# Kernel optimization log

Hardware: AMD Instinct MI355X
Metric: run time of the kernel (lower is better)

The kernel has to match this reference:

```python
import jax, jax.numpy as jnp
import numpy as np
import math

NUM_HEADS = 16
HIDDEN = 1024
MLP = 4096
SEQ = 2048
HEAD_DIM = HIDDEN // NUM_HEADS  # 64
EPS = 1e-5


def setup_inputs() -> dict:
    key = jax.random.key(0)
    ks = jax.random.split(key, 16)
    s = 0.02
    inp = {
        "x": jax.random.normal(ks[0], (SEQ, HIDDEN), jnp.float32),
        "rope_cos": jnp.cos(jnp.arange(SEQ, dtype=jnp.float32)[:, None] * (1.0 / (10000.0 ** (jnp.arange(HEAD_DIM // 2, dtype=jnp.float32) * 2 / HEAD_DIM)))[None, :]),
        "rope_sin": jnp.sin(jnp.arange(SEQ, dtype=jnp.float32)[:, None] * (1.0 / (10000.0 ** (jnp.arange(HEAD_DIM // 2, dtype=jnp.float32) * 2 / HEAD_DIM)))[None, :]),
        "norm0_w": jnp.ones((HIDDEN,), jnp.float32),
        "norm0_b": jnp.zeros((HIDDEN,), jnp.float32),
        "norm1_w": jnp.ones((HIDDEN,), jnp.float32),
        "norm1_b": jnp.zeros((HIDDEN,), jnp.float32),
        "wqkv_w": jax.random.normal(ks[1], (3 * HIDDEN, HIDDEN), jnp.float32) * s,
        "wqkv_b": jnp.zeros((3 * HIDDEN,), jnp.float32),
        "wo_w": jax.random.normal(ks[2], (HIDDEN, HIDDEN), jnp.float32) * s,
        "wo_b": jnp.zeros((HIDDEN,), jnp.float32),
        "up_w": jax.random.normal(ks[3], (MLP, HIDDEN), jnp.float32) * s,
        "up_b": jnp.zeros((MLP,), jnp.float32),
        "down_w": jax.random.normal(ks[4], (HIDDEN, MLP), jnp.float32) * s,
        "down_b": jnp.zeros((HIDDEN,), jnp.float32),
        # 4 packed sequences of length 512 each
        "input_row_offsets": jnp.array([0, 512, 1024, 1536, 2048], jnp.int32),
    }
    return inp


def _layernorm(x, w, b):
    m = jnp.mean(x, axis=-1, keepdims=True)
    v = jnp.mean((x - m) ** 2, axis=-1, keepdims=True)
    return (x - m) * jax.lax.rsqrt(v + EPS) * w + b


def _rope(t, cos, sin):
    # t: [S, nh, hd]; cos/sin: [S, hd/2] -> complex rotation of adjacent pairs
    S, nh, hd = t.shape
    t2 = t.reshape(S, nh, hd // 2, 2)
    re, im = t2[..., 0], t2[..., 1]
    c = cos[:, None, :]
    s = sin[:, None, :]
    out = jnp.stack([re * c - im * s, re * s + im * c], axis=-1)
    return out.reshape(S, nh, hd)


def _block(x, rope_cos, rope_sin, norm0_w, norm0_b, wqkv_w, wqkv_b, wo_w, wo_b,
           up_w, up_b, down_w, down_b, norm1_w, norm1_b, input_row_offsets):
    S, H = x.shape
    nh, hd = NUM_HEADS, HEAD_DIM
    h = _layernorm(x, norm0_w, norm0_b)
    qkv = (h @ wqkv_w.T + wqkv_b).reshape(S, 3, nh, hd)
    q, k, v = qkv[:, 0], qkv[:, 1], qkv[:, 2]
    q = _rope(q, rope_cos, rope_sin)
    k = _rope(k, rope_cos, rope_sin)
    # block-diagonal bool mask added as 0/1 float (matches torch `attn_weight += bool_mask`)
    seg = jnp.searchsorted(input_row_offsets, jnp.arange(S), side="right") - 1
    mask = (seg[:, None] == seg[None, :]).astype(jnp.float32)  # [S, S]
    scores = jnp.einsum("shd,thd->hst", q, k) / math.sqrt(hd) + mask[None]
    attn = jax.nn.softmax(scores.astype(jnp.float32), axis=-1).astype(q.dtype)
    out = jnp.einsum("hst,thd->shd", attn, v).reshape(S, H)
    x = x + (out @ wo_w.T + wo_b)
    h = _layernorm(x, norm1_w, norm1_b)
    h = jax.nn.gelu(h @ up_w.T + up_b, approximate=True)
    return x + (h @ down_w.T + down_b)


def reference(x, rope_cos, rope_sin, norm0_w, norm0_b, norm1_w, norm1_b,
              wqkv_w, wqkv_b, wo_w, wo_b, up_w, up_b, down_w, down_b,
              input_row_offsets):
    return _block(x, rope_cos, rope_sin, norm0_w, norm0_b, wqkv_w, wqkv_b,
                  wo_w, wo_b, up_w, up_b, down_w, down_b, norm1_w, norm1_b,
                  input_row_offsets)
```

## Files before the change

kernel.cpp:

```cpp
#include <hip/hip_runtime.h>
#include <hip/hip_bf16.h>
#include <math.h>

#define SEQ 2048
#define HID 1024
#define NH 16
#define HD 64

using f32x4  = __attribute__((ext_vector_type(4))) float;
using bf16x8 = __attribute__((ext_vector_type(8))) short;

union U8 { unsigned int u[4]; bf16x8 v; short s[8]; };

__device__ __forceinline__ short f2bf(float f) {
  unsigned int x = __float_as_uint(f);
  unsigned int r = (x + 0x7fffu + ((x >> 16) & 1u)) >> 16;
  return (short)(r & 0xffffu);
}

__device__ __forceinline__ unsigned int pkbf(float a, float b) {
  return ((unsigned int)(unsigned short)f2bf(a)) |
         (((unsigned int)(unsigned short)f2bf(b)) << 16);
}

__device__ __forceinline__ float bf2f_lo(unsigned int u) {
  return __uint_as_float((u & 0xffffu) << 16);
}
__device__ __forceinline__ float bf2f_hi(unsigned int u) {
  return __uint_as_float(u & 0xffff0000u);
}

__device__ __forceinline__ float fast_exp2(float x) {
#if __has_builtin(__builtin_amdgcn_exp2f)
  return __builtin_amdgcn_exp2f(x);
#else
  return exp2f(x);
#endif
}

__device__ __forceinline__ float fast_rcp(float x) {
#if __has_builtin(__builtin_amdgcn_rcpf)
  return __builtin_amdgcn_rcpf(x);
#else
  return 1.0f / x;
#endif
}

__device__ __forceinline__ void async_cp16(const void* g, void* l) {
  __builtin_amdgcn_global_load_lds(
      (__attribute__((address_space(1))) void*)(g),
      (__attribute__((address_space(3))) void*)(l), 16, 0, 0);
}

__global__ void cvt_all_kernel(const float* __restrict__ a, const float* __restrict__ b,
                               const float* __restrict__ c, const float* __restrict__ d,
                               short* __restrict__ oa, short* __restrict__ ob,
                               short* __restrict__ oc, short* __restrict__ od) {
  int i = blockIdx.x * blockDim.x + threadIdx.x;
  const float* src; short* dst; int off;
  if (i < 786432)        { src = a; dst = oa; off = i; }
  else if (i < 1048576)  { src = b; dst = ob; off = i - 786432; }
  else if (i < 2097152)  { src = c; dst = oc; off = i - 1048576; }
  else                   { src = d; dst = od; off = i - 2097152; }
  float4 v = ((const float4*)src)[off];
  short4 o;
  o.x = f2bf(v.x); o.y = f2bf(v.y); o.z = f2bf(v.z); o.w = f2bf(v.w);
  ((short4*)dst)[off] = o;
}

__global__ __launch_bounds__(256) void ln_kernel(const float* __restrict__ x,
    const float* __restrict__ w, const float* __restrict__ b, short* __restrict__ out) {
  int row = blockIdx.x;
  int tid = threadIdx.x;
  float4 v = ((const float4*)(x + (size_t)row * HID))[tid];
  float s  = v.x + v.y + v.z + v.w;
  float s2 = v.x*v.x + v.y*v.y + v.z*v.z + v.w*v.w;
#pragma unroll
  for (int o = 32; o >= 1; o >>= 1) {
    s  += __shfl_xor(s,  o);
    s2 += __shfl_xor(s2, o);
  }
  __shared__ float red[8];
  int wv = tid >> 6;
  if ((tid & 63) == 0) { red[wv] = s; red[4 + wv] = s2; }
  __syncthreads();
  float ts  = red[0] + red[1] + red[2] + red[3];
  float ts2 = red[4] + red[5] + red[6] + red[7];
  float mean = ts * (1.0f / HID);
  float var  = ts2 * (1.0f / HID) - mean * mean;
  float rs = rsqrtf(var + 1e-5f);
  float4 wv4 = ((const float4*)w)[tid];
  float4 bv4 = ((const float4*)b)[tid];
  short4 o;
  o.x = f2bf((v.x - mean) * rs * wv4.x + bv4.x);
  o.y = f2bf((v.y - mean) * rs * wv4.y + bv4.y);
  o.z = f2bf((v.z - mean) * rs * wv4.z + bv4.z);
  o.w = f2bf((v.w - mean) * rs * wv4.w + bv4.w);
  ((short4*)(out + (size_t)row * HID))[tid] = o;
}

__global__ __launch_bounds__(256) void ropev_kernel(const short* __restrict__ qkvb,
    const float* __restrict__ cosb, const float* __restrict__ sinb,
    short* __restrict__ Qh, short* __restrict__ Kh, short* __restrict__ Vt) {
  __shared__ short tile[64 * 72];
  int s0   = blockIdx.x * 64;
  int head = blockIdx.y;
  int tid  = threadIdx.x;
#pragma unroll
  for (int p = 0; p < 2; p++) {
    int seg = p * 256 + tid;
    int row = seg >> 3;
    int c8  = seg & 7;
    bf16x8 v = *(const bf16x8*)(qkvb + (size_t)(s0 + row) * 3072 + 2048 + head * 64 + c8 * 8);
    *(bf16x8*)(tile + row * 72 + c8 * 8) = v;
  }
  int sl = tid >> 3;
  int c  = tid & 7;
#pragma unroll
  for (int j = 0; j < 2; j++) {
    float scale = (j == 0) ? 0.18033688011112043f : 1.0f;
    short* dstm = (j == 0) ? Qh : Kh;
#pragma unroll
    for (int half = 0; half < 2; half++) {
      int s = s0 + half * 32 + sl;
      uint4 uu = *(const uint4*)(qkvb + (size_t)s * 3072 + j * 1024 + head * 64 + c * 8);
      float4 cs = *(const float4*)(cosb + s * 32 + c * 4);
      float4 sn = *(const float4*)(sinb + s * 32 + c * 4);
      uint4 oo;
      {
        float a = bf2f_lo(uu.x), b = bf2f_hi(uu.x);
        oo.x = pkbf(scale * (a * cs.x - b * sn.x), scale * (a * sn.x + b * cs.x));
        a = bf2f_lo(uu.y); b = bf2f_hi(uu.y);
        oo.y = pkbf(scale * (a * cs.y - b * sn.y), scale * (a * sn.y + b * cs.y));
        a = bf2f_lo(uu.z); b = bf2f_hi(uu.z);
        oo.z = pkbf(scale * (a * cs.z - b * sn.z), scale * (a * sn.z + b * cs.z));
        a = bf2f_lo(uu.w); b = bf2f_hi(uu.w);
        oo.w = pkbf(scale * (a * cs.w - b * sn.w), scale * (a * sn.w + b * cs.w));
      }
      *(uint4*)(dstm + ((size_t)head * SEQ + s) * HD + c * 8) = oo;
    }
  }
  __syncthreads();
#pragma unroll
  for (int p = 0; p < 2; p++) {
    int seg = p * 256 + tid;
    int d   = seg >> 3;
    int sc  = seg & 7;
    U8 o;
#pragma unroll
    for (int jj = 0; jj < 8; jj++) o.s[jj] = tile[(sc * 8 + jj) * 72 + d];
    *(bf16x8*)(Vt + ((size_t)head * HD + d) * SEQ + s0 + sc * 8) = o.v;
  }
}

template <int EPI>
__global__ __launch_bounds__(256) void gemm_bt_kernel(
    const short* __restrict__ A, const short* __restrict__ B,
    const float* __restrict__ bias, const float* __restrict__ resid,
    void* __restrict__ outp, int M, int N, int Klen, int Kstride) {
  __shared__ __attribute__((aligned(16))) short Alds[2 * 128 * 64];
  __shared__ __attribute__((aligned(16))) short Blds[2 * 128 * 64];
  int tid = threadIdx.x;
  int w    = tid >> 6;
  int lane = tid & 63;
  int lcol  = lane & 15;
  int lhalf = lane >> 4;
  int m0 = blockIdx.y * 128;
  int n0 = blockIdx.x * 128;
  int z  = blockIdx.z;
  int wm = (w & 1) * 64;
  int wn = (w >> 1) * 64;

  const short* apt[4];
  const short* bpt[4];
#pragma unroll
  for (int p = 0; p < 4; p++) {
    int seg = p * 256 + tid;
    int row = seg >> 3;
    int c   = (seg & 7) ^ (row & 7);
    apt[p] = A + (size_t)z * Klen + (size_t)(m0 + row) * Kstride + c * 8;
    bpt[p] = B + (size_t)z * Klen + (size_t)(n0 + row) * Kstride + c * 8;
  }

  f32x4 acc[4][4];
#pragma unroll
  for (int i = 0; i < 4; i++)
#pragma unroll
    for (int j = 0; j < 4; j++) acc[i][j] = (f32x4){0.f, 0.f, 0.f, 0.f};

  int nk = Klen >> 6;

#pragma unroll
  for (int p = 0; p < 4; p++) {
    async_cp16(apt[p], Alds + p * 2048 + w * 512);  apt[p] += 64;
    async_cp16(bpt[p], Blds + p * 2048 + w * 512);  bpt[p] += 64;
  }

  for (int kt = 0; kt < nk; ++kt) {
    int cur = kt & 1;
    const short* Ab = Alds + cur * 8192;
    const short* Bb = Blds + cur * 8192;
    if (kt + 1 < nk) {
      int nb = (cur ^ 1) * 8192;
#pragma unroll
      for (int p = 0; p < 4; p++) {
        async_cp16(apt[p], Alds + nb + p * 2048 + w * 512);  apt[p] += 64;
        async_cp16(bpt[p], Blds + nb + p * 2048 + w * 512);  bpt[p] += 64;
      }
      asm volatile("s_waitcnt vmcnt(8)" ::: "memory");
    } else {
      asm volatile("s_waitcnt vmcnt(0)" ::: "memory");
    }
    __builtin_amdgcn_s_barrier();
    __builtin_amdgcn_sched_barrier(0);
#pragma unroll
    for (int kc = 0; kc < 2; kc++) {
      bf16x8 af[4], bfr[4];
#pragma unroll
      for (int i = 0; i < 4; i++) {
        int row = wm + i * 16 + lcol;
        af[i] = *(const bf16x8*)(Ab + row * 64 + (((kc * 4 + lhalf) ^ (row & 7)) * 8));
      }
#pragma unroll
      for (int j = 0; j < 4; j++) {
        int row = wn + j * 16 + lcol;
        bfr[j] = *(const bf16x8*)(Bb + row * 64 + (((kc * 4 + lhalf) ^ (row & 7)) * 8));
      }
#pragma unroll
      for (int i = 0; i < 4; i++)
#pragma unroll
        for (int j = 0; j < 4; j++)
          acc[i][j] = __builtin_amdgcn_mfma_f32_16x16x32_bf16(af[i], bfr[j], acc[i][j], 0, 0, 0);
    }
    __builtin_amdgcn_s_barrier();
    __builtin_amdgcn_sched_barrier(0);
  }

#pragma unroll
  for (int i = 0; i < 4; i++) {
#pragma unroll
    for (int j = 0; j < 4; j++) {
#pragma unroll
      for (int r = 0; r < 4; r++) {
        int row = m0 + wm + i * 16 + lhalf * 4 + r;
        int col = n0 + wn + j * 16 + lcol;
        float v = acc[i][j][r];
        if (EPI != 5) v += bias[col];
        if (EPI == 2) {
          float t = v * (1.5957691216057308f + 0.07135481283942279f * v * v);
          float e = fast_exp2(t * -1.4426950408889634f);
          v = v * fast_rcp(1.0f + e);
          ((short*)outp)[(size_t)row * N + col] = f2bf(v);
        } else if (EPI == 3) {
          ((short*)outp)[(size_t)row * N + col] = f2bf(v);
        } else {
          ((short*)outp)[(size_t)z * M * N + (size_t)row * N + col] = f2bf(v);
        }
      }
    }
  }
}

__global__ __launch_bounds__(256) void attn_kernel(
    const short* __restrict__ Qh, const short* __restrict__ Kh,
    const short* __restrict__ Vt, const int* __restrict__ offs,
    short* __restrict__ Opart, float* __restrict__ Lpart) {
  __shared__ __attribute__((aligned(16))) short Klds[64 * 64];
  __shared__ __attribute__((aligned(16))) short Vlds[64 * 64];
  __shared__ __attribute__((aligned(16))) unsigned int Plds[4][16 * 34];
  int head = blockIdx.y;
  int q0   = blockIdx.x * 64;
  int z    = blockIdx.z;
  int tid  = threadIdx.x;
  int w    = tid >> 6;
  int lane = tid & 63;
  int lcol = lane & 15;
  int h    = lane >> 4;
  int s7   = lcol & 7;
  int o1 = offs[1], o2 = offs[2], o3 = offs[3];

  int qrow = q0 + w * 16 + lcol;
  const short* qb = Qh + ((size_t)head * SEQ + qrow) * HD;
  bf16x8 qf0 = *(const bf16x8*)(qb + h * 8);
  bf16x8 qf1 = *(const bf16x8*)(qb + 32 + h * 8);
  int sq = (qrow >= o1) + (qrow >= o2) + (qrow >= o3);
  U8 qe;
  qe.u[0] = 0; qe.u[1] = 0; qe.u[2] = 0; qe.u[3] = 0;
  if (h == 0) qe.s[sq] = (short)0x3FB9;

  bf16x8 ones;
#pragma unroll
  for (int i = 0; i < 8; i++) ones[i] = 0x3F80;

  int kb0 = lcol * 64 + ((h ^ s7) * 8);
  int kb1 = lcol * 64 + (((4 + h) ^ s7) * 8);
  int vb0 = kb0, vb1 = kb1;
  int pwb = lcol * 34 + h * 2;
  int prb = lcol * 34 + h * 4;

  int tbeg = z * 512;
  const short* kp0; const short* kp1; const short* vp0; const short* vp1;
  {
    int seg = tid, row = seg >> 3, g = (seg & 7) ^ (row & 7);
    kp0 = Kh + ((size_t)head * SEQ + tbeg + row) * HD + g * 8;
    vp0 = Vt + ((size_t)head * HD + row) * SEQ + tbeg + g * 8;
    seg = 256 + tid; row = seg >> 3; g = (seg & 7) ^ (row & 7);
    kp1 = Kh + ((size_t)head * SEQ + tbeg + row) * HD + g * 8;
    vp1 = Vt + ((size_t)head * HD + row) * SEQ + tbeg + g * 8;
  }

  f32x4 o_acc[4];
#pragma unroll
  for (int nt = 0; nt < 4; nt++) o_acc[nt] = (f32x4){0.f, 0.f, 0.f, 0.f};
  f32x4 acc_l = (f32x4){0.f, 0.f, 0.f, 0.f};

  for (int t0 = 0; t0 < 512; t0 += 64) {
    async_cp16(kp0, Klds + w * 512);          kp0 += 64 * HD;
    async_cp16(kp1, Klds + 2048 + w * 512);   kp1 += 64 * HD;
    async_cp16(vp0, Vlds + w * 512);          vp0 += 64;
    async_cp16(vp1, Vlds + 2048 + w * 512);   vp1 += 64;
    __syncthreads();

#pragma unroll
    for (int n = 0; n < 4; n++) {
      bf16x8 kf0 = *(const bf16x8*)(Klds + n * 1024 + kb0);
      bf16x8 kf1 = *(const bf16x8*)(Klds + n * 1024 + kb1);
      int key = tbeg + t0 + n * 16 + lcol;
      int sk = (key >= o1) + (key >= o2) + (key >= o3);
      U8 ke;
      ke.u[0] = (h == 0) ? ((sk == 0) ? 0x00003F80u : (sk == 1) ? 0x3F800000u : 0u) : 0u;
      ke.u[1] = (h == 0) ? ((sk == 2) ? 0x00003F80u : (sk == 3) ? 0x3F800000u : 0u) : 0u;
      ke.u[2] = 0; ke.u[3] = 0;

      f32x4 sacc = (f32x4){0.f, 0.f, 0.f, 0.f};
      sacc = __builtin_amdgcn_mfma_f32_16x16x32_bf16(kf0, qf0, sacc, 0, 0, 0);
      sacc = __builtin_amdgcn_mfma_f32_16x16x32_bf16(kf1, qf1, sacc, 0, 0, 0);
      sacc = __builtin_amdgcn_mfma_f32_16x16x32_bf16(ke.v, qe.v, sacc, 0, 0, 0);

      float p0 = fast_exp2(sacc[0]);
      float p1 = fast_exp2(sacc[1]);
      float p2 = fast_exp2(sacc[2]);
      float p3 = fast_exp2(sacc[3]);
      uint2 pw;
      pw.x = __builtin_amdgcn_perm(__float_as_uint(p1), __float_as_uint(p0), 0x07060302);
      pw.y = __builtin_amdgcn_perm(__float_as_uint(p3), __float_as_uint(p2), 0x07060302);
      *(uint2*)&Plds[w][pwb + n * 8] = pw;
    }

#pragma unroll
    for (int kc = 0; kc < 2; kc++) {
      uint2 a = *(const uint2*)&Plds[w][prb + kc * 16];
      uint2 b = *(const uint2*)&Plds[w][prb + kc * 16 + 2];
      U8 pu;
      pu.u[0] = a.x; pu.u[1] = a.y; pu.u[2] = b.x; pu.u[3] = b.y;
      int vb = kc ? vb1 : vb0;
#pragma unroll
      for (int nt = 0; nt < 4; nt++) {
        bf16x8 vf = *(const bf16x8*)(Vlds + nt * 1024 + vb);
        o_acc[nt] = __builtin_amdgcn_mfma_f32_16x16x32_bf16(vf, pu.v, o_acc[nt], 0, 0, 0);
      }
      acc_l = __builtin_amdgcn_mfma_f32_16x16x32_bf16(ones, pu.v, acc_l, 0, 0, 0);
    }
    __syncthreads();
  }

  short* op = Opart + ((size_t)z * SEQ + qrow) * HID + head * HD + h * 4;
#pragma unroll
  for (int nt = 0; nt < 4; nt++) {
    uint2 ua;
    ua.x = pkbf(o_acc[nt][0], o_acc[nt][1]);
    ua.y = pkbf(o_acc[nt][2], o_acc[nt][3]);
    *(uint2*)(op + nt * 16) = ua;
  }
  if (lane < 16)
    Lpart[((size_t)z * NH + head) * SEQ + qrow] = acc_l[0];
}

__global__ __launch_bounds__(256) void attn_merge_kernel(
    const short* __restrict__ Opart, const float* __restrict__ Lpart,
    short* __restrict__ attn) {
  int i = blockIdx.x * blockDim.x + threadIdx.x;
  int col4 = i & 255;
  int row  = i >> 8;
  int head = col4 >> 4;
  float acc0 = 0.f, acc1 = 0.f, acc2 = 0.f, acc3 = 0.f, l = 0.f;
#pragma unroll
  for (int zz = 0; zz < 4; zz++) {
    uint2 p = ((const uint2*)(Opart + (size_t)zz * SEQ * HID))[i];
    acc0 += bf2f_lo(p.x); acc1 += bf2f_hi(p.x);
    acc2 += bf2f_lo(p.y); acc3 += bf2f_hi(p.y);
    l += Lpart[((size_t)zz * NH + head) * SEQ + row];
  }
  float rl = fast_rcp(l);
  uint2 o;
  o.x = pkbf(acc0 * rl, acc1 * rl);
  o.y = pkbf(acc2 * rl, acc3 * rl);
  ((uint2*)attn)[i] = o;
}

__global__ __launch_bounds__(256) void merge_ln_kernel(
    const short* __restrict__ part, const float* __restrict__ bias,
    const float* __restrict__ resid, const float* __restrict__ w,
    const float* __restrict__ b, float* __restrict__ x1, short* __restrict__ h1) {
  int row = blockIdx.x;
  int tid = threadIdx.x;
  size_t idx = (size_t)row * HID / 4 + tid;
  float4 v = {0.f, 0.f, 0.f, 0.f};
#pragma unroll
  for (int z = 0; z < 4; z++) {
    uint2 p = ((const uint2*)(part + (size_t)z * SEQ * HID))[idx];
    v.x += bf2f_lo(p.x); v.y += bf2f_hi(p.x);
    v.z += bf2f_lo(p.y); v.w += bf2f_hi(p.y);
  }
  float4 bi = ((const float4*)bias)[tid];
  float4 rs4 = ((const float4*)(resid + (size_t)row * HID))[tid];
  v.x += bi.x + rs4.x; v.y += bi.y + rs4.y; v.z += bi.z + rs4.z; v.w += bi.w + rs4.w;
  ((float4*)(x1 + (size_t)row * HID))[tid] = v;
  float s  = v.x + v.y + v.z + v.w;
  float s2 = v.x*v.x + v.y*v.y + v.z*v.z + v.w*v.w;
#pragma unroll
  for (int o = 32; o >= 1; o >>= 1) {
    s  += __shfl_xor(s,  o);
    s2 += __shfl_xor(s2, o);
  }
  __shared__ float red[8];
  int wv = tid >> 6;
  if ((tid & 63) == 0) { red[wv] = s; red[4 + wv] = s2; }
  __syncthreads();
  float ts  = red[0] + red[1] + red[2] + red[3];
  float ts2 = red[4] + red[5] + red[6] + red[7];
  float mean = ts * (1.0f / HID);
  float var  = ts2 * (1.0f / HID) - mean * mean;
  float rsq = rsqrtf(var + 1e-5f);
  float4 wv4 = ((const float4*)w)[tid];
  float4 bv4 = ((const float4*)b)[tid];
  short4 o;
  o.x = f2bf((v.x - mean) * rsq * wv4.x + bv4.x);
  o.y = f2bf((v.y - mean) * rsq * wv4.y + bv4.y);
  o.z = f2bf((v.z - mean) * rsq * wv4.z + bv4.z);
  o.w = f2bf((v.w - mean) * rsq * wv4.w + bv4.w);
  ((short4*)(h1 + (size_t)row * HID))[tid] = o;
}

__global__ __launch_bounds__(256) void merge_bias_kernel(
    const short* __restrict__ part, const float* __restrict__ bias,
    const float* __restrict__ resid, float* __restrict__ out) {
  int i = blockIdx.x * blockDim.x + threadIdx.x;
  int col4 = i & 255;
  float4 v = {0.f, 0.f, 0.f, 0.f};
#pragma unroll
  for (int z = 0; z < 4; z++) {
    uint2 p = ((const uint2*)(part + (size_t)z * SEQ * HID))[i];
    v.x += bf2f_lo(p.x); v.y += bf2f_hi(p.x);
    v.z += bf2f_lo(p.y); v.w += bf2f_hi(p.y);
  }
  float4 bi = ((const float4*)bias)[col4];
  float4 rs = ((const float4*)resid)[i];
  float4 o;
  o.x = v.x + bi.x + rs.x;
  o.y = v.y + bi.y + rs.y;
  o.z = v.z + bi.z + rs.z;
  o.w = v.w + bi.w + rs.w;
  ((float4*)out)[i] = o;
}

extern "C" void kernel_launch(void* const* d_in, const int* in_sizes, int n_in,
                              void* d_out, int out_size, void* d_ws, size_t ws_size,
                              hipStream_t stream) {
  const float* x      = (const float*)d_in[0];
  const float* ropec  = (const float*)d_in[1];
  const float* ropes  = (const float*)d_in[2];
  const float* n0w    = (const float*)d_in[3];
  const float* n0b    = (const float*)d_in[4];
  const float* n1w    = (const float*)d_in[5];
  const float* n1b    = (const float*)d_in[6];
  const float* wqkv_w = (const float*)d_in[7];
  const float* wqkv_b = (const float*)d_in[8];
  const float* wo_w   = (const float*)d_in[9];
  const float* wo_b   = (const float*)d_in[10];
  const float* up_w   = (const float*)d_in[11];
  const float* up_b   = (const float*)d_in[12];
  const float* down_w = (const float*)d_in[13];
  const float* down_b = (const float*)d_in[14];
  const int*   offs   = (const int*)d_in[15];
  float* out = (float*)d_out;

  char* base = (char*)d_ws;
  short* wqkv_bf = (short*)(base + 0);
  short* wo_bf   = (short*)(base + 6291456);
  short* up_bf   = (short*)(base + 8388608);
  short* down_bf = (short*)(base + 16777216);
  short* h0      = (short*)(base + 25165824);
  short* qkv_bf  = (short*)(base + 29360128);
  short* Qh      = (short*)(base + 41943040);
  short* Kh      = (short*)(base + 46137344);
  short* Vt      = (short*)(base + 50331648);
  short* Opart   = (short*)(base + 54525952);
  float* Lpart   = (float*)(base + 71303168);
  short* attn    = (short*)(base + 71827456);
  float* x1      = (float*)(base + 76021760);
  short* h1      = (short*)(base + 84410368);
  short* wopart  = (short*)(base + 25165824);
  short* u       = (short*)(base + 25165824);
  short* dnpart  = (short*)(base + 41943040);

  cvt_all_kernel<<<12288, 256, 0, stream>>>(wqkv_w, wo_w, up_w, down_w,
                                            wqkv_bf, wo_bf, up_bf, down_bf);
  ln_kernel<<<2048, 256, 0, stream>>>(x, n0w, n0b, h0);
  gemm_bt_kernel<3><<<dim3(24, 16), 256, 0, stream>>>(h0, wqkv_bf, wqkv_b, nullptr,
                                                      qkv_bf, 2048, 3072, 1024, 1024);
  ropev_kernel<<<dim3(32, 16), 256, 0, stream>>>(qkv_bf, ropec, ropes, Qh, Kh, Vt);
  attn_kernel<<<dim3(32, 16, 4), 256, 0, stream>>>(Qh, Kh, Vt, offs, Opart, Lpart);
  attn_merge_kernel<<<2048, 256, 0, stream>>>(Opart, Lpart, attn);
  gemm_bt_kernel<5><<<dim3(8, 16, 4), 256, 0, stream>>>(attn, wo_bf, nullptr, nullptr,
                                                        wopart, 2048, 1024, 256, 1024);
  merge_ln_kernel<<<2048, 256, 0, stream>>>(wopart, wo_b, x, n1w, n1b, x1, h1);
  gemm_bt_kernel<2><<<dim3(32, 16), 256, 0, stream>>>(h1, up_bf, up_b, nullptr,
                                                      u, 2048, 4096, 1024, 1024);
  gemm_bt_kernel<5><<<dim3(8, 16, 4), 256, 0, stream>>>(u, down_bf, nullptr, nullptr,
                                                        dnpart, 2048, 1024, 1024, 4096);
  merge_bias_kernel<<<2048, 256, 0, stream>>>(dnpart, down_b, x1, out);
}
```

Before: 265.5 us.

## Split-K QKV/up/down GEMMs with single-buffer LDS, fuse LN into convert kernel

Merges the weight-conversion and first layernorm into a single launch. QKV, up and down projections switch to split-K (2 or 8 ways) with a single-buffered LDS variant for higher occupancy and more blocks. Bias, GELU and rope now consume the partial sums in the follow-on kernels, and a new merge_gelu kernel is added. This trades extra bf16 partial-sum traffic and an extra launch for more parallelism and less LDS per block, and loses the copy/compute overlap of double buffering in those GEMMs.

```diff
diff --git a/kernel.cpp b/kernel.cpp
--- a/kernel.cpp
+++ b/kernel.cpp
@@ -46,17 +46,56 @@
 #endif
 }
 
+__device__ __forceinline__ float gelu_f(float v) {
+  float t = v * (1.5957691216057308f + 0.07135481283942279f * v * v);
+  float e = fast_exp2(t * -1.4426950408889634f);
+  return v * fast_rcp(1.0f + e);
+}
+
 __device__ __forceinline__ void async_cp16(const void* g, void* l) {
   __builtin_amdgcn_global_load_lds(
       (__attribute__((address_space(1))) void*)(g),
       (__attribute__((address_space(3))) void*)(l), 16, 0, 0);
 }
 
-__global__ void cvt_all_kernel(const float* __restrict__ a, const float* __restrict__ b,
-                               const float* __restrict__ c, const float* __restrict__ d,
-                               short* __restrict__ oa, short* __restrict__ ob,
-                               short* __restrict__ oc, short* __restrict__ od) {
-  int i = blockIdx.x * blockDim.x + threadIdx.x;
+__global__ __launch_bounds__(256) void cvtln_kernel(
+    const float* __restrict__ a, const float* __restrict__ b,
+    const float* __restrict__ c, const float* __restrict__ d,
+    short* __restrict__ oa, short* __restrict__ ob,
+    short* __restrict__ oc, short* __restrict__ od,
+    const float* __restrict__ x, const float* __restrict__ w,
+    const float* __restrict__ bb, short* __restrict__ h0) {
+  int tid = threadIdx.x;
+  if (blockIdx.x < 2048) {
+    int row = blockIdx.x;
+    float4 v = ((const float4*)(x + (size_t)row * HID))[tid];
+    float s  = v.x + v.y + v.z + v.w;
+    float s2 = v.x*v.x + v.y*v.y + v.z*v.z + v.w*v.w;
+#pragma unroll
+    for (int o = 32; o >= 1; o >>= 1) {
+      s  += __shfl_xor(s,  o);
+      s2 += __shfl_xor(s2, o);
+    }
+    __shared__ float red[8];
+    int wv = tid >> 6;
+    if ((tid & 63) == 0) { red[wv] = s; red[4 + wv] = s2; }
+    __syncthreads();
+    float ts  = red[0] + red[1] + red[2] + red[3];
+    float ts2 = red[4] + red[5] + red[6] + red[7];
+    float mean = ts * (1.0f / HID);
+    float var  = ts2 * (1.0f / HID) - mean * mean;
+    float rs = rsqrtf(var + 1e-5f);
+    float4 wv4 = ((const float4*)w)[tid];
+    float4 bv4 = ((const float4*)bb)[tid];
+    short4 o;
+    o.x = f2bf((v.x - mean) * rs * wv4.x + bv4.x);
+    o.y = f2bf((v.y - mean) * rs * wv4.y + bv4.y);
+    o.z = f2bf((v.z - mean) * rs * wv4.z + bv4.z);
+    o.w = f2bf((v.w - mean) * rs * wv4.w + bv4.w);
+    ((short4*)(h0 + (size_t)row * HID))[tid] = o;
+    return;
+  }
+  int i = (blockIdx.x - 2048) * 256 + tid;
   const float* src; short* dst; int off;
   if (i < 786432)        { src = a; dst = oa; off = i; }
   else if (i < 1048576)  { src = b; dst = ob; off = i - 786432; }
@@ -68,41 +107,12 @@
   ((short4*)dst)[off] = o;
 }
 
-__global__ __launch_bounds__(256) void ln_kernel(const float* __restrict__ x,
-    const float* __restrict__ w, const float* __restrict__ b, short* __restrict__ out) {
-  int row = blockIdx.x;
-  int tid = threadIdx.x;
-  float4 v = ((const float4*)(x + (size_t)row * HID))[tid];
-  float s  = v.x + v.y + v.z + v.w;
-  float s2 = v.x*v.x + v.y*v.y + v.z*v.z + v.w*v.w;
-#pragma unroll
-  for (int o = 32; o >= 1; o >>= 1) {
-    s  += __shfl_xor(s,  o);
-    s2 += __shfl_xor(s2, o);
-  }
-  __shared__ float red[8];
-  int wv = tid >> 6;
-  if ((tid & 63) == 0) { red[wv] = s; red[4 + wv] = s2; }
-  __syncthreads();
-  float ts  = red[0] + red[1] + red[2] + red[3];
-  float ts2 = red[4] + red[5] + red[6] + red[7];
-  float mean = ts * (1.0f / HID);
-  float var  = ts2 * (1.0f / HID) - mean * mean;
-  float rs = rsqrtf(var + 1e-5f);
-  float4 wv4 = ((const float4*)w)[tid];
-  float4 bv4 = ((const float4*)b)[tid];
-  short4 o;
-  o.x = f2bf((v.x - mean) * rs * wv4.x + bv4.x);
-  o.y = f2bf((v.y - mean) * rs * wv4.y + bv4.y);
-  o.z = f2bf((v.z - mean) * rs * wv4.z + bv4.z);
-  o.w = f2bf((v.w - mean) * rs * wv4.w + bv4.w);
-  ((short4*)(out + (size_t)row * HID))[tid] = o;
-}
-
-__global__ __launch_bounds__(256) void ropev_kernel(const short* __restrict__ qkvb,
+__global__ __launch_bounds__(256) void ropev_kernel(const short* __restrict__ qkvp,
+    const float* __restrict__ qbias,
     const float* __restrict__ cosb, const float* __restrict__ sinb,
     short* __restrict__ Qh, short* __restrict__ Kh, short* __restrict__ Vt) {
   __shared__ short tile[64 * 72];
+  const size_t ZOFF = (size_t)SEQ * 3072;
   int s0   = blockIdx.x * 64;
   int head = blockIdx.y;
   int tid  = threadIdx.x;
@@ -111,8 +121,21 @@
     int seg = p * 256 + tid;
     int row = seg >> 3;
     int c8  = seg & 7;
-    bf16x8 v = *(const bf16x8*)(qkvb + (size_t)(s0 + row) * 3072 + 2048 + head * 64 + c8 * 8);
-    *(bf16x8*)(tile + row * 72 + c8 * 8) = v;
+    size_t off = (size_t)(s0 + row) * 3072 + 2048 + head * 64 + c8 * 8;
+    uint4 av = *(const uint4*)(qkvp + off);
+    uint4 bv = *(const uint4*)(qkvp + ZOFF + off);
+    float4 bi0 = *(const float4*)(qbias + 2048 + head * 64 + c8 * 8);
+    float4 bi1 = *(const float4*)(qbias + 2048 + head * 64 + c8 * 8 + 4);
+    U8 o;
+    o.u[0] = pkbf(bf2f_lo(av.x) + bf2f_lo(bv.x) + bi0.x,
+                  bf2f_hi(av.x) + bf2f_hi(bv.x) + bi0.y);
+    o.u[1] = pkbf(bf2f_lo(av.y) + bf2f_lo(bv.y) + bi0.z,
+                  bf2f_hi(av.y) + bf2f_hi(bv.y) + bi0.w);
+    o.u[2] = pkbf(bf2f_lo(av.z) + bf2f_lo(bv.z) + bi1.x,
+                  bf2f_hi(av.z) + bf2f_hi(bv.z) + bi1.y);
+    o.u[3] = pkbf(bf2f_lo(av.w) + bf2f_lo(bv.w) + bi1.z,
+                  bf2f_hi(av.w) + bf2f_hi(bv.w) + bi1.w);
+    *(bf16x8*)(tile + row * 72 + c8 * 8) = o.v;
   }
   int sl = tid >> 3;
   int c  = tid & 7;
@@ -123,20 +146,26 @@
 #pragma unroll
     for (int half = 0; half < 2; half++) {
       int s = s0 + half * 32 + sl;
-      uint4 uu = *(const uint4*)(qkvb + (size_t)s * 3072 + j * 1024 + head * 64 + c * 8);
+      size_t off = (size_t)s * 3072 + j * 1024 + head * 64 + c * 8;
+      uint4 av = *(const uint4*)(qkvp + off);
+      uint4 bv = *(const uint4*)(qkvp + ZOFF + off);
+      float4 bi0 = *(const float4*)(qbias + j * 1024 + head * 64 + c * 8);
+      float4 bi1 = *(const float4*)(qbias + j * 1024 + head * 64 + c * 8 + 4);
+      float e0 = bf2f_lo(av.x) + bf2f_lo(bv.x) + bi0.x;
+      float e1 = bf2f_hi(av.x) + bf2f_hi(bv.x) + bi0.y;
+      float e2 = bf2f_lo(av.y) + bf2f_lo(bv.y) + bi0.z;
+      float e3 = bf2f_hi(av.y) + bf2f_hi(bv.y) + bi0.w;
+      float e4 = bf2f_lo(av.z) + bf2f_lo(bv.z) + bi1.x;
+      float e5 = bf2f_hi(av.z) + bf2f_hi(bv.z) + bi1.y;
+      float e6 = bf2f_lo(av.w) + bf2f_lo(bv.w) + bi1.z;
+      float e7 = bf2f_hi(av.w) + bf2f_hi(bv.w) + bi1.w;
       float4 cs = *(const float4*)(cosb + s * 32 + c * 4);
       float4 sn = *(const float4*)(sinb + s * 32 + c * 4);
       uint4 oo;
-      {
-        float a = bf2f_lo(uu.x), b = bf2f_hi(uu.x);
-        oo.x = pkbf(scale * (a * cs.x - b * sn.x), scale * (a * sn.x + b * cs.x));
-        a = bf2f_lo(uu.y); b = bf2f_hi(uu.y);
-        oo.y = pkbf(scale * (a * cs.y - b * sn.y), scale * (a * sn.y + b * cs.y));
-        a = bf2f_lo(uu.z); b = bf2f_hi(uu.z);
-        oo.z = pkbf(scale * (a * cs.z - b * sn.z), scale * (a * sn.z + b * cs.z));
-        a = bf2f_lo(uu.w); b = bf2f_hi(uu.w);
-        oo.w = pkbf(scale * (a * cs.w - b * sn.w), scale * (a * sn.w + b * cs.w));
-      }
+      oo.x = pkbf(scale * (e0 * cs.x - e1 * sn.x), scale * (e0 * sn.x + e1 * cs.x));
+      oo.y = pkbf(scale * (e2 * cs.y - e3 * sn.y), scale * (e2 * sn.y + e3 * cs.y));
+      oo.z = pkbf(scale * (e4 * cs.z - e5 * sn.z), scale * (e4 * sn.z + e5 * cs.z));
+      oo.w = pkbf(scale * (e6 * cs.w - e7 * sn.w), scale * (e6 * sn.w + e7 * cs.w));
       *(uint4*)(dstm + ((size_t)head * SEQ + s) * HD + c * 8) = oo;
     }
   }
@@ -153,13 +182,13 @@
   }
 }
 
-template <int EPI>
+template <int EPI, bool DBUF>
 __global__ __launch_bounds__(256) void gemm_bt_kernel(
     const short* __restrict__ A, const short* __restrict__ B,
     const float* __restrict__ bias, const float* __restrict__ resid,
     void* __restrict__ outp, int M, int N, int Klen, int Kstride) {
-  __shared__ __attribute__((aligned(16))) short Alds[2 * 128 * 64];
-  __shared__ __attribute__((aligned(16))) short Blds[2 * 128 * 64];
+  __shared__ __attribute__((aligned(16))) short Alds[(DBUF ? 2 : 1) * 128 * 64];
+  __shared__ __attribute__((aligned(16))) short Blds[(DBUF ? 2 : 1) * 128 * 64];
   int tid = threadIdx.x;
   int w    = tid >> 6;
   int lane = tid & 63;
@@ -188,52 +217,81 @@
 #pragma unroll
     for (int j = 0; j < 4; j++) acc[i][j] = (f32x4){0.f, 0.f, 0.f, 0.f};
 
-  int nk = Klen >> 6;
-
-#pragma unroll
-  for (int p = 0; p < 4; p++) {
-    async_cp16(apt[p], Alds + p * 2048 + w * 512);  apt[p] += 64;
-    async_cp16(bpt[p], Blds + p * 2048 + w * 512);  bpt[p] += 64;
-  }
-
-  for (int kt = 0; kt < nk; ++kt) {
-    int cur = kt & 1;
-    const short* Ab = Alds + cur * 8192;
-    const short* Bb = Blds + cur * 8192;
-    if (kt + 1 < nk) {
-      int nb = (cur ^ 1) * 8192;
+  if constexpr (DBUF) {
+    int nk = Klen >> 6;
+#pragma unroll
+    for (int p = 0; p < 4; p++) {
+      async_cp16(apt[p], Alds + p * 2048 + w * 512);  apt[p] += 64;
+      async_cp16(bpt[p], Blds + p * 2048 + w * 512);  bpt[p] += 64;
+    }
+    for (int kt = 0; kt < nk; ++kt) {
+      int cur = kt & 1;
+      const short* Ab = Alds + cur * 8192;
+      const short* Bb = Blds + cur * 8192;
+      if (kt + 1 < nk) {
+        int nb = (cur ^ 1) * 8192;
+#pragma unroll
+        for (int p = 0; p < 4; p++) {
+          async_cp16(apt[p], Alds + nb + p * 2048 + w * 512);  apt[p] += 64;
+          async_cp16(bpt[p], Blds + nb + p * 2048 + w * 512);  bpt[p] += 64;
+        }
+        asm volatile("s_waitcnt vmcnt(8)" ::: "memory");
+      } else {
+        asm volatile("s_waitcnt vmcnt(0)" ::: "memory");
+      }
+      __builtin_amdgcn_s_barrier();
+      __builtin_amdgcn_sched_barrier(0);
+#pragma unroll
+      for (int kc = 0; kc < 2; kc++) {
+        bf16x8 af[4], bfr[4];
+#pragma unroll
+        for (int i = 0; i < 4; i++) {
+          int row = wm + i * 16 + lcol;
+          af[i] = *(const bf16x8*)(Ab + row * 64 + (((kc * 4 + lhalf) ^ (row & 7)) * 8));
+        }
+#pragma unroll
+        for (int j = 0; j < 4; j++) {
+          int row = wn + j * 16 + lcol;
+          bfr[j] = *(const bf16x8*)(Bb + row * 64 + (((kc * 4 + lhalf) ^ (row & 7)) * 8));
+        }
+#pragma unroll
+        for (int i = 0; i < 4; i++)
+#pragma unroll
+          for (int j = 0; j < 4; j++)
+            acc[i][j] = __builtin_amdgcn_mfma_f32_16x16x32_bf16(af[i], bfr[j], acc[i][j], 0, 0, 0);
+      }
+      __builtin_amdgcn_s_barrier();
+      __builtin_amdgcn_sched_barrier(0);
+    }
+  } else {
+    for (int k0 = 0; k0 < Klen; k0 += 64) {
 #pragma unroll
       for (int p = 0; p < 4; p++) {
-        async_cp16(apt[p], Alds + nb + p * 2048 + w * 512);  apt[p] += 64;
-        async_cp16(bpt[p], Blds + nb + p * 2048 + w * 512);  bpt[p] += 64;
+        async_cp16(apt[p], Alds + p * 2048 + w * 512);  apt[p] += 64;
+        async_cp16(bpt[p], Blds + p * 2048 + w * 512);  bpt[p] += 64;
       }
-      asm volatile("s_waitcnt vmcnt(8)" ::: "memory");
-    } else {
-      asm volatile("s_waitcnt vmcnt(0)" ::: "memory");
-    }
-    __builtin_amdgcn_s_barrier();
-    __builtin_amdgcn_sched_barrier(0);
-#pragma unroll
-    for (int kc = 0; kc < 2; kc++) {
-      bf16x8 af[4], bfr[4];
-#pragma unroll
-      for (int i = 0; i < 4; i++) {
-        int row = wm + i * 16 + lcol;
-        af[i] = *(const bf16x8*)(Ab + row * 64 + (((kc * 4 + lhalf) ^ (row & 7)) * 8));
+      __syncthreads();
+#pragma unroll
+      for (int kc = 0; kc < 2; kc++) {
+        bf16x8 af[4], bfr[4];
+#pragma unroll
+        for (int i = 0; i < 4; i++) {
+          int row = wm + i * 16 + lcol;
+          af[i] = *(const bf16x8*)(Alds + row * 64 + (((kc * 4 + lhalf) ^ (row & 7)) * 8));
+        }
+#pragma unroll
+        for (int j = 0; j < 4; j++) {
+          int row = wn + j * 16 + lcol;
+          bfr[j] = *(const bf16x8*)(Blds + row * 64 + (((kc * 4 + lhalf) ^ (row & 7)) * 8));
+        }
+#pragma unroll
+        for (int i = 0; i < 4; i++)
+#pragma unroll
+          for (int j = 0; j < 4; j++)
+            acc[i][j] = __builtin_amdgcn_mfma_f32_16x16x32_bf16(af[i], bfr[j], acc[i][j], 0, 0, 0);
       }
-#pragma unroll
-      for (int j = 0; j < 4; j++) {
-        int row = wn + j * 16 + lcol;
-        bfr[j] = *(const bf16x8*)(Bb + row * 64 + (((kc * 4 + lhalf) ^ (row & 7)) * 8));
-      }
-#pragma unroll
-      for (int i = 0; i < 4; i++)
-#pragma unroll
-        for (int j = 0; j < 4; j++)
-          acc[i][j] = __builtin_amdgcn_mfma_f32_16x16x32_bf16(af[i], bfr[j], acc[i][j], 0, 0, 0);
-    }
-    __builtin_amdgcn_s_barrier();
-    __builtin_amdgcn_sched_barrier(0);
+      __syncthreads();
+    }
   }
 
 #pragma unroll
@@ -247,9 +305,7 @@
         float v = acc[i][j][r];
         if (EPI != 5) v += bias[col];
         if (EPI == 2) {
-          float t = v * (1.5957691216057308f + 0.07135481283942279f * v * v);
-          float e = fast_exp2(t * -1.4426950408889634f);
-          v = v * fast_rcp(1.0f + e);
+          v = gelu_f(v);
           ((short*)outp)[(size_t)row * N + col] = f2bf(v);
         } else if (EPI == 3) {
           ((short*)outp)[(size_t)row * N + col] = f2bf(v);
@@ -442,6 +498,24 @@
   ((short4*)(h1 + (size_t)row * HID))[tid] = o;
 }
 
+__global__ __launch_bounds__(256) void merge_gelu_kernel(
+    const short* __restrict__ part, const float* __restrict__ bias,
+    short* __restrict__ u) {
+  int i = blockIdx.x * 256 + threadIdx.x;
+  int col4 = i & 1023;
+  uint2 p0 = ((const uint2*)part)[i];
+  uint2 p1 = ((const uint2*)(part + (size_t)SEQ * 4096))[i];
+  float4 bi = ((const float4*)bias)[col4];
+  float v0 = bf2f_lo(p0.x) + bf2f_lo(p1.x) + bi.x;
+  float v1 = bf2f_hi(p0.x) + bf2f_hi(p1.x) + bi.y;
+  float v2 = bf2f_lo(p0.y) + bf2f_lo(p1.y) + bi.z;
+  float v3 = bf2f_hi(p0.y) + bf2f_hi(p1.y) + bi.w;
+  uint2 o;
+  o.x = pkbf(gelu_f(v0), gelu_f(v1));
+  o.y = pkbf(gelu_f(v2), gelu_f(v3));
+  ((uint2*)u)[i] = o;
+}
+
 __global__ __launch_bounds__(256) void merge_bias_kernel(
     const short* __restrict__ part, const float* __restrict__ bias,
     const float* __restrict__ resid, float* __restrict__ out) {
@@ -449,7 +523,7 @@
   int col4 = i & 255;
   float4 v = {0.f, 0.f, 0.f, 0.f};
 #pragma unroll
-  for (int z = 0; z < 4; z++) {
+  for (int z = 0; z < 8; z++) {
     uint2 p = ((const uint2*)(part + (size_t)z * SEQ * HID))[i];
     v.x += bf2f_lo(p.x); v.y += bf2f_hi(p.x);
     v.z += bf2f_lo(p.y); v.w += bf2f_hi(p.y);
@@ -491,33 +565,36 @@
   short* up_bf   = (short*)(base + 8388608);
   short* down_bf = (short*)(base + 16777216);
   short* h0      = (short*)(base + 25165824);
-  short* qkv_bf  = (short*)(base + 29360128);
-  short* Qh      = (short*)(base + 41943040);
-  short* Kh      = (short*)(base + 46137344);
-  short* Vt      = (short*)(base + 50331648);
-  short* Opart   = (short*)(base + 54525952);
-  float* Lpart   = (float*)(base + 71303168);
-  short* attn    = (short*)(base + 71827456);
-  float* x1      = (float*)(base + 76021760);
-  short* h1      = (short*)(base + 84410368);
+  short* qkvpart = (short*)(base + 29360128);
+  short* Qh      = (short*)(base + 54525952);
+  short* Kh      = (short*)(base + 58720256);
+  short* Vt      = (short*)(base + 62914560);
+  short* Opart   = (short*)(base + 67108864);
+  float* Lpart   = (float*)(base + 83886080);
+  short* attn    = (short*)(base + 84410368);
+  float* x1      = (float*)(base + 88604672);
+  short* h1      = (short*)(base + 96993280);
   short* wopart  = (short*)(base + 25165824);
-  short* u       = (short*)(base + 25165824);
-  short* dnpart  = (short*)(base + 41943040);
-
-  cvt_all_kernel<<<12288, 256, 0, stream>>>(wqkv_w, wo_w, up_w, down_w,
-                                            wqkv_bf, wo_bf, up_bf, down_bf);
-  ln_kernel<<<2048, 256, 0, stream>>>(x, n0w, n0b, h0);
-  gemm_bt_kernel<3><<<dim3(24, 16), 256, 0, stream>>>(h0, wqkv_bf, wqkv_b, nullptr,
-                                                      qkv_bf, 2048, 3072, 1024, 1024);
-  ropev_kernel<<<dim3(32, 16), 256, 0, stream>>>(qkv_bf, ropec, ropes, Qh, Kh, Vt);
+  short* upart   = (short*)(base + 25165824);
+  short* u       = (short*)(base + 58720256);
+  short* dnpart  = (short*)(base + 25165824);
+
+  cvtln_kernel<<<14336, 256, 0, stream>>>(wqkv_w, wo_w, up_w, down_w,
+                                          wqkv_bf, wo_bf, up_bf, down_bf,
+                                          x, n0w, n0b, h0);
+  gemm_bt_kernel<5, false><<<dim3(24, 16, 2), 256, 0, stream>>>(
+      h0, wqkv_bf, nullptr, nullptr, qkvpart, 2048, 3072, 512, 1024);
+  ropev_kernel<<<dim3(32, 16), 256, 0, stream>>>(qkvpart, wqkv_b, ropec, ropes,
+                                                 Qh, Kh, Vt);
   attn_kernel<<<dim3(32, 16, 4), 256, 0, stream>>>(Qh, Kh, Vt, offs, Opart, Lpart);
   attn_merge_kernel<<<2048, 256, 0, stream>>>(Opart, Lpart, attn);
-  gemm_bt_kernel<5><<<dim3(8, 16, 4), 256, 0, stream>>>(attn, wo_bf, nullptr, nullptr,
-                                                        wopart, 2048, 1024, 256, 1024);
+  gemm_bt_kernel<5, true><<<dim3(8, 16, 4), 256, 0, stream>>>(
+      attn, wo_bf, nullptr, nullptr, wopart, 2048, 1024, 256, 1024);
   merge_ln_kernel<<<2048, 256, 0, stream>>>(wopart, wo_b, x, n1w, n1b, x1, h1);
-  gemm_bt_kernel<2><<<dim3(32, 16), 256, 0, stream>>>(h1, up_bf, up_b, nullptr,
-                                                      u, 2048, 4096, 1024, 1024);
-  gemm_bt_kernel<5><<<dim3(8, 16, 4), 256, 0, stream>>>(u, down_bf, nullptr, nullptr,
-                                                        dnpart, 2048, 1024, 1024, 4096);
+  gemm_bt_kernel<5, false><<<dim3(32, 16, 2), 256, 0, stream>>>(
+      h1, up_bf, nullptr, nullptr, upart, 2048, 4096, 512, 1024);
+  merge_gelu_kernel<<<8192, 256, 0, stream>>>(upart, up_b, u);
+  gemm_bt_kernel<5, false><<<dim3(8, 16, 8), 256, 0, stream>>>(
+      u, down_bf, nullptr, nullptr, dnpart, 2048, 1024, 512, 4096);
   merge_bias_kernel<<<2048, 256, 0, stream>>>(dnpart, down_b, x1, out);
 }
```

New measurement: 285.4 us. 1.07x slower.

## Fuse weight conversion with first layernorm; widen attention blocks to 128 queries

Applied to the files above, without the earlier changes.

Merges the bf16 weight-conversion kernel and the first layernorm into a single launch, using the first 2048 blocks for layernorm rows and the rest for conversion. This removes one kernel launch and its serialization gap. The attention kernel now runs 512 threads (8 waves) per block covering 128 queries, so each K/V tile loaded into LDS is shared by twice as many query rows and each thread issues one async copy per tile instead of two. The trade-off is half as many attention blocks, with more LDS and registers per block, which may lower occupancy.

```diff
diff --git a/kernel.cpp b/kernel.cpp
--- a/kernel.cpp
+++ b/kernel.cpp
@@ -46,17 +46,56 @@
 #endif
 }
 
+__device__ __forceinline__ float gelu_f(float v) {
+  float t = v * (1.5957691216057308f + 0.07135481283942279f * v * v);
+  float e = fast_exp2(t * -1.4426950408889634f);
+  return v * fast_rcp(1.0f + e);
+}
+
 __device__ __forceinline__ void async_cp16(const void* g, void* l) {
   __builtin_amdgcn_global_load_lds(
       (__attribute__((address_space(1))) void*)(g),
       (__attribute__((address_space(3))) void*)(l), 16, 0, 0);
 }
 
-__global__ void cvt_all_kernel(const float* __restrict__ a, const float* __restrict__ b,
-                               const float* __restrict__ c, const float* __restrict__ d,
-                               short* __restrict__ oa, short* __restrict__ ob,
-                               short* __restrict__ oc, short* __restrict__ od) {
-  int i = blockIdx.x * blockDim.x + threadIdx.x;
+__global__ __launch_bounds__(256) void cvtln_kernel(
+    const float* __restrict__ a, const float* __restrict__ b,
+    const float* __restrict__ c, const float* __restrict__ d,
+    short* __restrict__ oa, short* __restrict__ ob,
+    short* __restrict__ oc, short* __restrict__ od,
+    const float* __restrict__ x, const float* __restrict__ w,
+    const float* __restrict__ bb, short* __restrict__ h0) {
+  int tid = threadIdx.x;
+  if (blockIdx.x < 2048) {
+    int row = blockIdx.x;
+    float4 v = ((const float4*)(x + (size_t)row * HID))[tid];
+    float s  = v.x + v.y + v.z + v.w;
+    float s2 = v.x*v.x + v.y*v.y + v.z*v.z + v.w*v.w;
+#pragma unroll
+    for (int o = 32; o >= 1; o >>= 1) {
+      s  += __shfl_xor(s,  o);
+      s2 += __shfl_xor(s2, o);
+    }
+    __shared__ float red[8];
+    int wv = tid >> 6;
+    if ((tid & 63) == 0) { red[wv] = s; red[4 + wv] = s2; }
+    __syncthreads();
+    float ts  = red[0] + red[1] + red[2] + red[3];
+    float ts2 = red[4] + red[5] + red[6] + red[7];
+    float mean = ts * (1.0f / HID);
+    float var  = ts2 * (1.0f / HID) - mean * mean;
+    float rs = rsqrtf(var + 1e-5f);
+    float4 wv4 = ((const float4*)w)[tid];
+    float4 bv4 = ((const float4*)bb)[tid];
+    short4 o;
+    o.x = f2bf((v.x - mean) * rs * wv4.x + bv4.x);
+    o.y = f2bf((v.y - mean) * rs * wv4.y + bv4.y);
+    o.z = f2bf((v.z - mean) * rs * wv4.z + bv4.z);
+    o.w = f2bf((v.w - mean) * rs * wv4.w + bv4.w);
+    ((short4*)(h0 + (size_t)row * HID))[tid] = o;
+    return;
+  }
+  int i = (blockIdx.x - 2048) * 256 + tid;
   const float* src; short* dst; int off;
   if (i < 786432)        { src = a; dst = oa; off = i; }
   else if (i < 1048576)  { src = b; dst = ob; off = i - 786432; }
@@ -66,37 +105,6 @@
   short4 o;
   o.x = f2bf(v.x); o.y = f2bf(v.y); o.z = f2bf(v.z); o.w = f2bf(v.w);
   ((short4*)dst)[off] = o;
-}
-
-__global__ __launch_bounds__(256) void ln_kernel(const float* __restrict__ x,
-    const float* __restrict__ w, const float* __restrict__ b, short* __restrict__ out) {
-  int row = blockIdx.x;
-  int tid = threadIdx.x;
-  float4 v = ((const float4*)(x + (size_t)row * HID))[tid];
-  float s  = v.x + v.y + v.z + v.w;
-  float s2 = v.x*v.x + v.y*v.y + v.z*v.z + v.w*v.w;
-#pragma unroll
-  for (int o = 32; o >= 1; o >>= 1) {
-    s  += __shfl_xor(s,  o);
-    s2 += __shfl_xor(s2, o);
-  }
-  __shared__ float red[8];
-  int wv = tid >> 6;
-  if ((tid & 63) == 0) { red[wv] = s; red[4 + wv] = s2; }
-  __syncthreads();
-  float ts  = red[0] + red[1] + red[2] + red[3];
-  float ts2 = red[4] + red[5] + red[6] + red[7];
-  float mean = ts * (1.0f / HID);
-  float var  = ts2 * (1.0f / HID) - mean * mean;
-  float rs = rsqrtf(var + 1e-5f);
-  float4 wv4 = ((const float4*)w)[tid];
-  float4 bv4 = ((const float4*)b)[tid];
-  short4 o;
-  o.x = f2bf((v.x - mean) * rs * wv4.x + bv4.x);
-  o.y = f2bf((v.y - mean) * rs * wv4.y + bv4.y);
-  o.z = f2bf((v.z - mean) * rs * wv4.z + bv4.z);
-  o.w = f2bf((v.w - mean) * rs * wv4.w + bv4.w);
-  ((short4*)(out + (size_t)row * HID))[tid] = o;
 }
 
 __global__ __launch_bounds__(256) void ropev_kernel(const short* __restrict__ qkvb,
@@ -189,13 +197,11 @@
     for (int j = 0; j < 4; j++) acc[i][j] = (f32x4){0.f, 0.f, 0.f, 0.f};
 
   int nk = Klen >> 6;
-
 #pragma unroll
   for (int p = 0; p < 4; p++) {
     async_cp16(apt[p], Alds + p * 2048 + w * 512);  apt[p] += 64;
     async_cp16(bpt[p], Blds + p * 2048 + w * 512);  bpt[p] += 64;
   }
-
   for (int kt = 0; kt < nk; ++kt) {
     int cur = kt & 1;
     const short* Ab = Alds + cur * 8192;
@@ -247,9 +253,7 @@
         float v = acc[i][j][r];
         if (EPI != 5) v += bias[col];
         if (EPI == 2) {
-          float t = v * (1.5957691216057308f + 0.07135481283942279f * v * v);
-          float e = fast_exp2(t * -1.4426950408889634f);
-          v = v * fast_rcp(1.0f + e);
+          v = gelu_f(v);
           ((short*)outp)[(size_t)row * N + col] = f2bf(v);
         } else if (EPI == 3) {
           ((short*)outp)[(size_t)row * N + col] = f2bf(v);
@@ -261,15 +265,15 @@
   }
 }
 
-__global__ __launch_bounds__(256) void attn_kernel(
+__global__ __launch_bounds__(512) void attn_kernel(
     const short* __restrict__ Qh, const short* __restrict__ Kh,
     const short* __restrict__ Vt, const int* __restrict__ offs,
     short* __restrict__ Opart, float* __restrict__ Lpart) {
   __shared__ __attribute__((aligned(16))) short Klds[64 * 64];
   __shared__ __attribute__((aligned(16))) short Vlds[64 * 64];
-  __shared__ __attribute__((aligned(16))) unsigned int Plds[4][16 * 34];
+  __shared__ __attribute__((aligned(16))) unsigned int Plds[8][16 * 34];
   int head = blockIdx.y;
-  int q0   = blockIdx.x * 64;
+  int q0   = blockIdx.x * 128;
   int z    = blockIdx.z;
   int tid  = threadIdx.x;
   int w    = tid >> 6;
@@ -299,14 +303,11 @@
   int prb = lcol * 34 + h * 4;
 
   int tbeg = z * 512;
-  const short* kp0; const short* kp1; const short* vp0; const short* vp1;
+  const short* kp; const short* vp;
   {
-    int seg = tid, row = seg >> 3, g = (seg & 7) ^ (row & 7);
-    kp0 = Kh + ((size_t)head * SEQ + tbeg + row) * HD + g * 8;
-    vp0 = Vt + ((size_t)head * HD + row) * SEQ + tbeg + g * 8;
-    seg = 256 + tid; row = seg >> 3; g = (seg & 7) ^ (row & 7);
-    kp1 = Kh + ((size_t)head * SEQ + tbeg + row) * HD + g * 8;
-    vp1 = Vt + ((size_t)head * HD + row) * SEQ + tbeg + g * 8;
+    int row = tid >> 3, g = (tid & 7) ^ (row & 7);
+    kp = Kh + ((size_t)head * SEQ + tbeg + row) * HD + g * 8;
+    vp = Vt + ((size_t)head * HD + row) * SEQ + tbeg + g * 8;
   }
 
   f32x4 o_acc[4];
@@ -315,10 +316,8 @@
   f32x4 acc_l = (f32x4){0.f, 0.f, 0.f, 0.f};
 
   for (int t0 = 0; t0 < 512; t0 += 64) {
-    async_cp16(kp0, Klds + w * 512);          kp0 += 64 * HD;
-    async_cp16(kp1, Klds + 2048 + w * 512);   kp1 += 64 * HD;
-    async_cp16(vp0, Vlds + w * 512);          vp0 += 64;
-    async_cp16(vp1, Vlds + 2048 + w * 512);   vp1 += 64;
+    async_cp16(kp, Klds + w * 512);   kp += 64 * HD;
+    async_cp16(vp, Vlds + w * 512);   vp += 64;
     __syncthreads();
 
 #pragma unroll
@@ -504,13 +503,13 @@
   short* u       = (short*)(base + 25165824);
   short* dnpart  = (short*)(base + 41943040);
 
-  cvt_all_kernel<<<12288, 256, 0, stream>>>(wqkv_w, wo_w, up_w, down_w,
-                                            wqkv_bf, wo_bf, up_bf, down_bf);
-  ln_kernel<<<2048, 256, 0, stream>>>(x, n0w, n0b, h0);
+  cvtln_kernel<<<14336, 256, 0, stream>>>(wqkv_w, wo_w, up_w, down_w,
+                                          wqkv_bf, wo_bf, up_bf, down_bf,
+                                          x, n0w, n0b, h0);
   gemm_bt_kernel<3><<<dim3(24, 16), 256, 0, stream>>>(h0, wqkv_bf, wqkv_b, nullptr,
                                                       qkv_bf, 2048, 3072, 1024, 1024);
   ropev_kernel<<<dim3(32, 16), 256, 0, stream>>>(qkv_bf, ropec, ropes, Qh, Kh, Vt);
-  attn_kernel<<<dim3(32, 16, 4), 256, 0, stream>>>(Qh, Kh, Vt, offs, Opart, Lpart);
+  attn_kernel<<<dim3(16, 16, 4), 512, 0, stream>>>(Qh, Kh, Vt, offs, Opart, Lpart);
   attn_merge_kernel<<<2048, 256, 0, stream>>>(Opart, Lpart, attn);
   gemm_bt_kernel<5><<<dim3(8, 16, 4), 256, 0, stream>>>(attn, wo_bf, nullptr, nullptr,
                                                         wopart, 2048, 1024, 256, 1024);
```

Result: no change. 265.5 us (+0.0%).
